# Kernel tuning notes

Measured on AMD Instinct MI355X. Metric: run time of the kernel, lower is better.

Reference implementation:

```python
import jax, jax.numpy as jnp
import numpy as np

THRESHOLD = 0.01
TOPK_RATIO = 0.7

def setup_inputs() -> dict:
    key = jax.random.key(0)
    k1, k2, k3, k4, k5 = jax.random.split(key, 5)
    B, N, F, K = 8, 2048, 512, 256
    x = jax.random.normal(k1, (B, N, F), dtype=jnp.float32)
    adj = jax.random.uniform(k2, (B, N, N), dtype=jnp.float32)
    mask = jnp.ones((B, N), dtype=jnp.float32)
    # assign_main = Linear(F->K), ReLU, Linear(K->K)
    W1 = jax.random.normal(k3, (F, K), dtype=jnp.float32) / np.sqrt(F)
    b1 = jnp.zeros((K,), dtype=jnp.float32)
    W2 = jax.random.normal(k4, (K, K), dtype=jnp.float32) / np.sqrt(K)
    b2 = jnp.zeros((K,), dtype=jnp.float32)
    return {"x": x, "adj": adj, "mask": mask, "W1": W1, "b1": b1, "W2": W2, "b2": b2}

def reference(x, adj, mask, W1, b1, W2, b2):
    B, N, Fdim = x.shape
    K = W2.shape[1]
    # soft assignment logits with masked softmax over clusters
    h = jax.nn.relu(jnp.einsum('bnf,fk->bnk', x, W1) + b1)
    logits = jnp.einsum('bnk,kl->bnl', h, W2) + b2            # [B,N,K]
    logits = logits + (-1e9) * (1.0 - mask[..., None])
    S = jax.nn.softmax(logits, axis=-1)                       # [B,N,K]
    # pooled features and pooled adjacency
    pfeat = jnp.einsum('bnk,bnf->bkf', S, x)                  # S^T x -> [B,K,F]
    mid = jnp.einsum('bnm,bmk->bnk', adj, S)                  # adj @ S
    pooled = jnp.einsum('bnk,bnl->bkl', S, mid)               # S^T adj S -> [B,K,K]
    # threshold + top-k sparsify with straight-through estimator
    topk = min(K, int(np.ceil(TOPK_RATIO * K)))
    thr_mask = (pooled >= THRESHOLD).astype(pooled.dtype)
    a_thr = pooled * thr_mask
    _, idx = jax.lax.top_k(a_thr, topk)                       # [B,K,topk]
    bi = jnp.arange(B)[:, None, None]
    ri = jnp.arange(K)[None, :, None]
    fmask = jnp.zeros_like(pooled).at[bi, ri, idx].set(1.0)
    a_sp = pooled * fmask
    a_ste = a_sp + jax.lax.stop_gradient(pooled - a_sp)       # forward == pooled
    # symmetric degree renormalization
    row_sum = a_ste.sum(axis=-1)
    d_inv_sqrt = 1.0 / jnp.sqrt(row_sum + 1e-9)
    pooled_adj = a_ste * d_inv_sqrt[:, :, None] * d_inv_sqrt[:, None, :]
    pmask = jnp.ones((B, K), dtype=x.dtype)
    return pfeat, pooled_adj, pmask
```

## Files before the change

kernel.cpp:

```cpp
#include <hip/hip_runtime.h>
#include <hip/hip_bf16.h>


typedef float f32x4 __attribute__((ext_vector_type(4)));
typedef __bf16 bf16x8 __attribute__((ext_vector_type(8)));

#define VMCNT(n) asm volatile("s_waitcnt vmcnt(" #n ")" ::: "memory")
#define LGKM0    asm volatile("s_waitcnt lgkmcnt(0)" ::: "memory")
#define SCHEDB   __builtin_amdgcn_sched_barrier(0)
#define BARRIER                                        \
  do {                                                 \
    LGKM0;                                             \
    __builtin_amdgcn_s_barrier();                      \
    asm volatile("" ::: "memory");                     \
    SCHEDB;                                            \
  } while (0)

__device__ __forceinline__ void async_load16(const void* g, void* l) {
  __builtin_amdgcn_global_load_lds((const __attribute__((address_space(1))) void*)g,
                                   (__attribute__((address_space(3))) void*)l, 16, 0, 0);
}
__device__ __forceinline__ unsigned short f2bf(float f) {
  return __builtin_bit_cast(unsigned short, (__bf16)f);
}
__device__ __forceinline__ ushort4 f4_to_bf4(float4 v) {
  ushort4 u; u.x = f2bf(v.x); u.y = f2bf(v.y); u.z = f2bf(v.z); u.w = f2bf(v.w); return u;
}

template <int ROWS, int BK, int NT>
__device__ __forceinline__ void stage_bf16(const __bf16* __restrict__ src, long long ld,
                                           __bf16* lds, int t) {
  constexpr int GR = BK / 8;
  constexpr int N = ROWS * GR / NT;
  static_assert(N >= 1, "stage too small");
#pragma unroll
  for (int c = 0; c < N; ++c) {
    const int idx = c * NT + t;
    const int row = idx / GR;
    const int g = idx % GR;
    const int gs = g ^ (row & (GR - 1) & 7);
    async_load16(src + (long long)row * ld + gs * 8, lds + idx * 8);
  }
}
template <int BK>
__device__ __forceinline__ bf16x8 frag(const __bf16* lds, int row, int kq) {
  constexpr int GR = BK / 8;
  const int g = kq ^ (row & (GR - 1) & 7);
  return *(const bf16x8*)(lds + row * BK + g * 8);
}

__global__ __launch_bounds__(256) void prep_k(const float* __restrict__ x,
                                              const float* __restrict__ W1,
                                              const float* __restrict__ W2,
                                              __bf16* __restrict__ xbT,
                                              __bf16* __restrict__ W1T,
                                              __bf16* __restrict__ W2T) {
  __shared__ float tile[64][65];
  const int tr = threadIdx.x >> 6, tc = threadIdx.x & 63;
  const int bid = blockIdx.x;
  const float* in; __bf16* out; int r0, c0, C, R;
  if (bid < 2048) {
    const int fb = bid >> 8, rest = bid & 255;
    const int nb = rest >> 3, b = rest & 7;
    in = x + (long long)b * 1048576; out = xbT + (long long)b * 1048576;
    r0 = nb * 64; c0 = fb * 64; R = 2048; C = 512;
  } else if (bid < 2080) {
    const int w = bid - 2048;
    in = W1; out = W1T; r0 = (w >> 2) * 64; c0 = (w & 3) * 64; R = 512; C = 256;
  } else {
    const int w = bid - 2080;
    in = W2; out = W2T; r0 = (w >> 2) * 64; c0 = (w & 3) * 64; R = 256; C = 256;
  }
#pragma unroll
  for (int i = 0; i < 16; ++i)
    tile[tr + i * 4][tc] = in[(long long)(r0 + tr + i * 4) * C + c0 + tc];
  __syncthreads();
#pragma unroll
  for (int i = 0; i < 16; ++i)
    out[(long long)(c0 + tr + i * 4) * R + r0 + tc] = (__bf16)tile[tc][tr + i * 4];
}

__device__ __forceinline__ void asg_compute(const __bf16* __restrict__ Abuf,
                                            const __bf16* __restrict__ Bbuf,
                                            f32x4 (&acc)[2][4], int wn, int l15, int l4) {
  bf16x8 af[2], bf[4];
#pragma unroll
  for (int i = 0; i < 2; ++i) af[i] = frag<32>(Abuf, i * 16 + l15, l4);
#pragma unroll
  for (int j = 0; j < 4; ++j) bf[j] = frag<32>(Bbuf, wn + j * 16 + l15, l4);
  __builtin_amdgcn_s_setprio(1);
#pragma unroll
  for (int i = 0; i < 2; ++i)
#pragma unroll
    for (int j = 0; j < 4; ++j)
      acc[i][j] = __builtin_amdgcn_mfma_f32_16x16x32_bf16(af[i], bf[j], acc[i][j], 0, 0, 0);
  __builtin_amdgcn_s_setprio(0);
}

__global__ __launch_bounds__(256) void assign_fused_k(
    const float* __restrict__ x, const __bf16* __restrict__ W1T,
    const __bf16* __restrict__ W2T, const float* __restrict__ b1,
    const float* __restrict__ b2, const float* __restrict__ mask,
    __bf16* __restrict__ ST) {
  __shared__ alignas(16) __bf16 Ax[2][32 * 32];
  __shared__ alignas(16) __bf16 Bw[2][256 * 32];
  __shared__ alignas(16) __bf16 hl[32 * 264];
  __shared__ float red[2][4][32];

  const int t = threadIdx.x;
  const int lane = t & 63, wave = t >> 6;
  const int l15 = lane & 15, l4 = lane >> 4;
  const int wn = wave * 64;
  const long long row0 = (long long)blockIdx.x * 32;
  const float* Xb = x + row0 * 512;

  const int arow = t >> 3, afq = t & 7;
  const int ag = afq >> 1;
  const int aoff = arow * 32 + ((ag ^ (arow & 3)) * 8) + (afq & 1) * 4;

  auto ldx = [&](int tile) -> float4 {
    return *(const float4*)(Xb + (long long)arow * 512 + tile * 32 + afq * 4);
  };
  auto sta = [&](__bf16* dst, float4 v) { *(ushort4*)&dst[aoff] = f4_to_bf4(v); };

  f32x4 acc[2][4] = {};

  float4 xA = ldx(0);
  SCHEDB;
  stage_bf16<256, 32, 256>(W1T, 512, Bw[0], t);
  SCHEDB;
  VMCNT(4); SCHEDB;
  sta(Ax[0], xA);
  float4 xB = ldx(1);
  SCHEDB;
  VMCNT(1); SCHEDB;
  BARRIER;

#pragma unroll 1
  for (int tt = 0; tt < 14; tt += 2) {
    stage_bf16<256, 32, 256>(W1T + (tt + 1) * 32, 512, Bw[1], t);
    SCHEDB;
    xA = ldx(tt + 2);
    SCHEDB;
    asg_compute(Ax[0], Bw[0], acc, wn, l15, l4);
    VMCNT(5); SCHEDB;
    sta(Ax[1], xB);
    VMCNT(1); SCHEDB;
    BARRIER;
    stage_bf16<256, 32, 256>(W1T + (tt + 2) * 32, 512, Bw[0], t);
    SCHEDB;
    xB = ldx(tt + 3);
    SCHEDB;
    asg_compute(Ax[1], Bw[1], acc, wn, l15, l4);
    VMCNT(5); SCHEDB;
    sta(Ax[0], xA);
    VMCNT(1); SCHEDB;
    BARRIER;
  }
  stage_bf16<256, 32, 256>(W1T + 15 * 32, 512, Bw[1], t);
  SCHEDB;
  asg_compute(Ax[0], Bw[0], acc, wn, l15, l4);
  VMCNT(4); SCHEDB;
  sta(Ax[1], xB);
  VMCNT(0); SCHEDB;
  BARRIER;
  asg_compute(Ax[1], Bw[1], acc, wn, l15, l4);

  stage_bf16<256, 32, 256>(W2T, 256, Bw[0], t);
  SCHEDB;
#pragma unroll
  for (int j = 0; j < 4; ++j) {
    const int col = wn + j * 16 + l15;
    const float bv = b1[col];
#pragma unroll
    for (int i = 0; i < 2; ++i)
#pragma unroll
      for (int r = 0; r < 4; ++r)
        hl[(i * 16 + l4 * 4 + r) * 264 + col] = (__bf16)fmaxf(acc[i][j][r] + bv, 0.f);
  }
  VMCNT(0); SCHEDB;
  BARRIER;

  f32x4 acc2[2][4] = {};
#pragma unroll 1
  for (int tt = 0; tt < 8; ++tt) {
    if (tt < 7) stage_bf16<256, 32, 256>(W2T + (tt + 1) * 32, 256, Bw[(tt & 1) ^ 1], t);
    SCHEDB;
    const __bf16* Bc = Bw[tt & 1];
    bf16x8 af[2], bf[4];
#pragma unroll
    for (int i = 0; i < 2; ++i)
      af[i] = *(const bf16x8*)(&hl[(i * 16 + l15) * 264 + tt * 32 + l4 * 8]);
#pragma unroll
    for (int j = 0; j < 4; ++j) bf[j] = frag<32>(Bc, wn + j * 16 + l15, l4);
#pragma unroll
    for (int i = 0; i < 2; ++i)
#pragma unroll
      for (int j = 0; j < 4; ++j)
        acc2[i][j] = __builtin_amdgcn_mfma_f32_16x16x32_bf16(af[i], bf[j], acc2[i][j], 0, 0, 0);
    VMCNT(0); SCHEDB;
    BARRIER;
  }

  float mb[2][4], mx[2][4], sm[2][4];
#pragma unroll
  for (int i = 0; i < 2; ++i)
#pragma unroll
    for (int r = 0; r < 4; ++r) {
      mb[i][r] = -1e9f * (1.0f - mask[row0 + i * 16 + l4 * 4 + r]);
      mx[i][r] = -3.4e38f;
      sm[i][r] = 0.f;
    }
#pragma unroll
  for (int j = 0; j < 4; ++j) {
    const float bv = b2[wn + j * 16 + l15];
#pragma unroll
    for (int i = 0; i < 2; ++i)
#pragma unroll
      for (int r = 0; r < 4; ++r) {
        const float v = acc2[i][j][r] + bv + mb[i][r];
        acc2[i][j][r] = v;
        mx[i][r] = fmaxf(mx[i][r], v);
      }
  }
#pragma unroll
  for (int i = 0; i < 2; ++i)
#pragma unroll
    for (int r = 0; r < 4; ++r) {
      float m = mx[i][r];
      m = fmaxf(m, __shfl_xor(m, 1, 64)); m = fmaxf(m, __shfl_xor(m, 2, 64));
      m = fmaxf(m, __shfl_xor(m, 4, 64)); m = fmaxf(m, __shfl_xor(m, 8, 64));
      mx[i][r] = m;
    }
  if (l15 == 0)
#pragma unroll
    for (int i = 0; i < 2; ++i)
#pragma unroll
      for (int r = 0; r < 4; ++r) red[0][wave][i * 16 + l4 * 4 + r] = mx[i][r];
  __syncthreads();
#pragma unroll
  for (int i = 0; i < 2; ++i)
#pragma unroll
    for (int r = 0; r < 4; ++r) {
      const int rl = i * 16 + l4 * 4 + r;
      mx[i][r] = fmaxf(fmaxf(red[0][0][rl], red[0][1][rl]),
                       fmaxf(red[0][2][rl], red[0][3][rl]));
    }
#pragma unroll
  for (int j = 0; j < 4; ++j)
#pragma unroll
    for (int i = 0; i < 2; ++i)
#pragma unroll
      for (int r = 0; r < 4; ++r) {
        const float e = __expf(acc2[i][j][r] - mx[i][r]);
        acc2[i][j][r] = e;
        sm[i][r] += e;
      }
#pragma unroll
  for (int i = 0; i < 2; ++i)
#pragma unroll
    for (int r = 0; r < 4; ++r) {
      float s = sm[i][r];
      s += __shfl_xor(s, 1, 64); s += __shfl_xor(s, 2, 64);
      s += __shfl_xor(s, 4, 64); s += __shfl_xor(s, 8, 64);
      sm[i][r] = s;
    }
  if (l15 == 0)
#pragma unroll
    for (int i = 0; i < 2; ++i)
#pragma unroll
      for (int r = 0; r < 4; ++r) red[1][wave][i * 16 + l4 * 4 + r] = sm[i][r];
  __syncthreads();
  float inv[2][4];
#pragma unroll
  for (int i = 0; i < 2; ++i)
#pragma unroll
    for (int r = 0; r < 4; ++r) {
      const int rl = i * 16 + l4 * 4 + r;
      inv[i][r] = 1.0f / (red[1][0][rl] + red[1][1][rl] + red[1][2][rl] + red[1][3][rl]);
    }
  const long long bb = row0 >> 11;
  const long long n0 = row0 & 2047;
  __bf16* Sb = ST + bb * 524288;
#pragma unroll
  for (int j = 0; j < 4; ++j) {
    const int col = wn + j * 16 + l15;
#pragma unroll
    for (int i = 0; i < 2; ++i) {
      ushort4 u;
      u.x = f2bf(acc2[i][j][0] * inv[i][0]);
      u.y = f2bf(acc2[i][j][1] * inv[i][1]);
      u.z = f2bf(acc2[i][j][2] * inv[i][2]);
      u.w = f2bf(acc2[i][j][3] * inv[i][3]);
      *(ushort4*)(Sb + (long long)col * 2048 + n0 + i * 16 + l4 * 4) = u;
    }
  }
}

__device__ __forceinline__ void adj_compute(const __bf16* __restrict__ Abuf,
                                            const __bf16* __restrict__ Bbuf,
                                            f32x4 (&acc)[2][4],
                                            int wn, int l15, int l4) {
#pragma unroll
  for (int ks = 0; ks < 2; ++ks) {
    bf16x8 af[2], bf[4];
#pragma unroll
    for (int i = 0; i < 2; ++i) af[i] = frag<64>(Abuf, i * 16 + l15, ks * 4 + l4);
#pragma unroll
    for (int j = 0; j < 4; ++j) bf[j] = frag<64>(Bbuf, wn + j * 16 + l15, ks * 4 + l4);
    __builtin_amdgcn_s_setprio(1);
#pragma unroll
    for (int i = 0; i < 2; ++i)
#pragma unroll
      for (int j = 0; j < 4; ++j)
        acc[i][j] = __builtin_amdgcn_mfma_f32_16x16x32_bf16(af[i], bf[j], acc[i][j], 0, 0, 0);
    __builtin_amdgcn_s_setprio(0);
  }
}

__global__ __launch_bounds__(256) void gemm_adj_k(const float* __restrict__ adj,
                                                  const __bf16* __restrict__ ST,
                                                  __bf16* __restrict__ midT) {
  __shared__ alignas(16) __bf16 Aa[2][32 * 64];
  __shared__ alignas(16) __bf16 Bs[2][256 * 64];
  const int t = threadIdx.x;
  const int lane = t & 63, wave = t >> 6;
  const int l15 = lane & 15, l4 = lane >> 4;
  const int wn = wave * 64;
  const int id = blockIdx.x;
  const int bz = id & 7;
  const long long r0 = (long long)(id >> 3) * 32;
  const float* Ab = adj + (long long)bz * 4194304 + r0 * 2048;
  const __bf16* Bb = ST + (long long)bz * 524288;

  const int arow = t >> 4, afq = t & 15;
  const int ag = afq >> 1;
  const int aoff0 = arow * 64 + ((ag ^ (arow & 7)) * 8) + (afq & 1) * 4;
  const int aoff1 = (arow + 16) * 64 + ((ag ^ ((arow + 16) & 7)) * 8) + (afq & 1) * 4;

  auto lda4 = [&](int tile, int half) -> float4 {
    return *(const float4*)(Ab + (long long)(arow + half * 16) * 2048 + tile * 64 + afq * 4);
  };
  auto sta = [&](__bf16* dst, float4 v0, float4 v1) {
    *(ushort4*)&dst[aoff0] = f4_to_bf4(v0);
    *(ushort4*)&dst[aoff1] = f4_to_bf4(v1);
  };

  f32x4 acc[2][4] = {};

  float4 aA0 = lda4(0, 0), aA1 = lda4(0, 1);
  SCHEDB;
  stage_bf16<256, 64, 256>(Bb, 2048, Bs[0], t);
  SCHEDB;
  VMCNT(8); SCHEDB;
  sta(Aa[0], aA0, aA1);
  float4 aB0 = lda4(1, 0), aB1 = lda4(1, 1);
  SCHEDB;
  VMCNT(2); SCHEDB;
  BARRIER;

#pragma unroll 1
  for (int tt = 0; tt < 30; tt += 2) {
    stage_bf16<256, 64, 256>(Bb + (tt + 1) * 64, 2048, Bs[1], t);
    SCHEDB;
    aA0 = lda4(tt + 2, 0); aA1 = lda4(tt + 2, 1);
    SCHEDB;
    adj_compute(Aa[0], Bs[0], acc, wn, l15, l4);
    VMCNT(10); SCHEDB;
    sta(Aa[1], aB0, aB1);
    VMCNT(2); SCHEDB;
    BARRIER;
    stage_bf16<256, 64, 256>(Bb + (tt + 2) * 64, 2048, Bs[0], t);
    SCHEDB;
    aB0 = lda4(tt + 3, 0); aB1 = lda4(tt + 3, 1);
    SCHEDB;
    adj_compute(Aa[1], Bs[1], acc, wn, l15, l4);
    VMCNT(10); SCHEDB;
    sta(Aa[0], aA0, aA1);
    VMCNT(2); SCHEDB;
    BARRIER;
  }
  stage_bf16<256, 64, 256>(Bb + 31 * 64, 2048, Bs[1], t);
  SCHEDB;
  adj_compute(Aa[0], Bs[0], acc, wn, l15, l4);
  VMCNT(8); SCHEDB;
  sta(Aa[1], aB0, aB1);
  VMCNT(0); SCHEDB;
  BARRIER;
  adj_compute(Aa[1], Bs[1], acc, wn, l15, l4);

  __bf16* Cb = midT + (long long)bz * 524288;
#pragma unroll
  for (int j = 0; j < 4; ++j) {
    const int l = wn + j * 16 + l15;
#pragma unroll
    for (int i = 0; i < 2; ++i) {
      ushort4 u;
      u.x = f2bf(acc[i][j][0]); u.y = f2bf(acc[i][j][1]);
      u.z = f2bf(acc[i][j][2]); u.w = f2bf(acc[i][j][3]);
      *(ushort4*)(Cb + (long long)l * 2048 + r0 + i * 16 + l4 * 4) = u;
    }
  }
}

__global__ __launch_bounds__(256) void gemm_feat_k(const __bf16* __restrict__ ST,
                                                   const __bf16* __restrict__ xbT,
                                                   float* __restrict__ pfeat) {
  __shared__ alignas(16) __bf16 As[2][32 * 64];
  __shared__ alignas(16) __bf16 Bs[2][64 * 64];
  const int t = threadIdx.x;
  const int lane = t & 63, wave = t >> 6;
  const int l15 = lane & 15, l4 = lane >> 4;
  const int wn = wave * 16;
  const int id = blockIdx.x;
  const int b = id & 7, j7 = id >> 3;
  const int kblk = j7 & 7, fblk = j7 >> 3;
  const __bf16* Ab = ST + (long long)b * 524288 + (long long)kblk * 32 * 2048;
  const __bf16* Bb = xbT + (long long)b * 1048576 + (long long)fblk * 64 * 2048;

  f32x4 acc[2] = {};
  stage_bf16<32, 64, 256>(Ab, 2048, As[0], t);
  stage_bf16<64, 64, 256>(Bb, 2048, Bs[0], t);
  __syncthreads();
#pragma unroll 1
  for (int tt = 0; tt < 32; ++tt) {
    const int cur = tt & 1;
    if (tt < 31) {
      stage_bf16<32, 64, 256>(Ab + (tt + 1) * 64, 2048, As[cur ^ 1], t);
      stage_bf16<64, 64, 256>(Bb + (tt + 1) * 64, 2048, Bs[cur ^ 1], t);
    }
#pragma unroll
    for (int ks = 0; ks < 2; ++ks) {
      bf16x8 af[2], bf;
#pragma unroll
      for (int i = 0; i < 2; ++i) af[i] = frag<64>(As[cur], i * 16 + l15, ks * 4 + l4);
      bf = frag<64>(Bs[cur], wn + l15, ks * 4 + l4);
#pragma unroll
      for (int i = 0; i < 2; ++i)
        acc[i] = __builtin_amdgcn_mfma_f32_16x16x32_bf16(af[i], bf, acc[i], 0, 0, 0);
    }
    __syncthreads();
  }
  float* out = pfeat + (long long)b * 131072;
#pragma unroll
  for (int i = 0; i < 2; ++i)
#pragma unroll
    for (int r = 0; r < 4; ++r)
      out[(long long)(kblk * 32 + i * 16 + l4 * 4 + r) * 512 + fblk * 64 + wn + l15] =
          acc[i][r];
}

__global__ __launch_bounds__(256) void gemm_pool_k(const __bf16* __restrict__ ST,
                                                   const __bf16* __restrict__ midT,
                                                   float* __restrict__ pooled) {
  __shared__ alignas(16) __bf16 As[2][32 * 64];
  __shared__ alignas(16) __bf16 Bs[2][32 * 64];
  const int t = threadIdx.x;
  const int lane = t & 63, wave = t >> 6;
  const int l15 = lane & 15, l4 = lane >> 4;
  const int wm = (wave >> 1) * 16, wn = (wave & 1) * 16;
  const int id = blockIdx.x;
  const int b = id & 7, j7 = id >> 3;
  const int kblk = j7 & 7, lblk = j7 >> 3;
  const __bf16* Ab = ST + (long long)b * 524288 + (long long)kblk * 32 * 2048;
  const __bf16* Bb = midT + (long long)b * 524288 + (long long)lblk * 32 * 2048;

  f32x4 acc = {};
  stage_bf16<32, 64, 256>(Ab, 2048, As[0], t);
  stage_bf16<32, 64, 256>(Bb, 2048, Bs[0], t);
  __syncthreads();
#pragma unroll 1
  for (int tt = 0; tt < 32; ++tt) {
    const int cur = tt & 1;
    if (tt < 31) {
      stage_bf16<32, 64, 256>(Ab + (tt + 1) * 64, 2048, As[cur ^ 1], t);
      stage_bf16<32, 64, 256>(Bb + (tt + 1) * 64, 2048, Bs[cur ^ 1], t);
    }
#pragma unroll
    for (int ks = 0; ks < 2; ++ks) {
      bf16x8 af = frag<64>(As[cur], wm + l15, ks * 4 + l4);
      bf16x8 bf = frag<64>(Bs[cur], wn + l15, ks * 4 + l4);
      acc = __builtin_amdgcn_mfma_f32_16x16x32_bf16(af, bf, acc, 0, 0, 0);
    }
    __syncthreads();
  }
  float* out = pooled + (long long)b * 65536;
#pragma unroll
  for (int r = 0; r < 4; ++r)
    out[(long long)(kblk * 32 + wm + l4 * 4 + r) * 256 + lblk * 32 + wn + l15] = acc[r];
}

__global__ __launch_bounds__(256) void rowsum_k(const float* __restrict__ pooled,
                                                float* __restrict__ dinv) {
  const int gr = blockIdx.x * 4 + (threadIdx.x >> 6);
  const int lane = threadIdx.x & 63;
  const float* p = pooled + (long long)gr * 256;
  float s = p[lane] + p[lane + 64] + p[lane + 128] + p[lane + 192];
#pragma unroll
  for (int o = 32; o > 0; o >>= 1) s += __shfl_xor(s, o, 64);
  if (lane == 0) dinv[gr] = rsqrtf(s + 1e-9f);
}

__global__ __launch_bounds__(256) void finalize_k(const float* __restrict__ pooled,
                                                  const float* __restrict__ dinv,
                                                  float* __restrict__ outAdj,
                                                  float* __restrict__ pmask) {
  const long long i = blockIdx.x * 256LL + threadIdx.x;
  const int c = (int)(i & 255);
  const int r = (int)((i >> 8) & 255);
  const int b = (int)(i >> 16);
  outAdj[i] = pooled[i] * dinv[b * 256 + r] * dinv[b * 256 + c];
  if (i < 2048) pmask[i] = 1.0f;
}

extern "C" void kernel_launch(void* const* d_in, const int* in_sizes, int n_in,
                              void* d_out, int out_size, void* d_ws, size_t ws_size,
                              hipStream_t stream) {
  (void)in_sizes; (void)n_in; (void)out_size; (void)ws_size;
  const float* x    = (const float*)d_in[0];
  const float* adj  = (const float*)d_in[1];
  const float* mask = (const float*)d_in[2];
  const float* W1   = (const float*)d_in[3];
  const float* b1   = (const float*)d_in[4];
  const float* W2   = (const float*)d_in[5];
  const float* b2   = (const float*)d_in[6];

  char* ws = (char*)d_ws;
  __bf16* ST     = (__bf16*)(ws + 0);
  __bf16* midT   = (__bf16*)(ws + 8388608);
  __bf16* xbT    = (__bf16*)(ws + 16777216);
  float*  pooled = (float*)(ws + 33554432);
  float*  dinv   = (float*)(ws + 35651584);
  __bf16* W1T    = (__bf16*)(ws + 35659776);
  __bf16* W2T    = (__bf16*)(ws + 35921920);

  float* pfeat  = (float*)d_out;
  float* outAdj = (float*)d_out + 1048576;
  float* pmask  = (float*)d_out + 1572864;

  prep_k<<<2096, 256, 0, stream>>>(x, W1, W2, xbT, W1T, W2T);
  assign_fused_k<<<512, 256, 0, stream>>>(x, W1T, W2T, b1, b2, mask, ST);
  gemm_feat_k<<<512, 256, 0, stream>>>(ST, xbT, pfeat);
  gemm_adj_k<<<512, 256, 0, stream>>>(adj, ST, midT);
  gemm_pool_k<<<512, 256, 0, stream>>>(ST, midT, pooled);
  rowsum_k<<<512, 256, 0, stream>>>(pooled, dinv);
  finalize_k<<<2048, 256, 0, stream>>>(pooled, dinv, outAdj, pmask);
}
```

Before: 113.4 us.

## Load adj GEMM B operand straight to registers; triple-buffer feat and pool GEMMs

In the adj@S kernel, the shared-memory staging of the 256x64 S tile is removed. Each wave now loads its B fragments straight from global memory into registers, double-buffered, and the wait and barrier order is adjusted. This cuts LDS traffic and shared-memory footprint, which could raise occupancy, but it adds register pressure and uncoalesced 16-byte global loads. The pfeat and pooled GEMM kernels move from double to triple LDS buffering, with vmcnt-based waits and fewer barriers, so loads run further ahead of compute.

```diff
diff --git a/kernel.cpp b/kernel.cpp
--- a/kernel.cpp
+++ b/kernel.cpp
@@ -297,23 +297,21 @@
   }
 }
 
-__device__ __forceinline__ void adj_compute(const __bf16* __restrict__ Abuf,
-                                            const __bf16* __restrict__ Bbuf,
-                                            f32x4 (&acc)[2][4],
-                                            int wn, int l15, int l4) {
+__device__ __forceinline__ void adj_cmp(const __bf16* __restrict__ Abuf,
+                                        const bf16x8* __restrict__ bq,
+                                        f32x4 (&acc)[2][4], int l15, int l4) {
 #pragma unroll
   for (int ks = 0; ks < 2; ++ks) {
-    bf16x8 af[2], bf[4];
+    bf16x8 af[2];
 #pragma unroll
     for (int i = 0; i < 2; ++i) af[i] = frag<64>(Abuf, i * 16 + l15, ks * 4 + l4);
-#pragma unroll
-    for (int j = 0; j < 4; ++j) bf[j] = frag<64>(Bbuf, wn + j * 16 + l15, ks * 4 + l4);
     __builtin_amdgcn_s_setprio(1);
 #pragma unroll
     for (int i = 0; i < 2; ++i)
 #pragma unroll
       for (int j = 0; j < 4; ++j)
-        acc[i][j] = __builtin_amdgcn_mfma_f32_16x16x32_bf16(af[i], bf[j], acc[i][j], 0, 0, 0);
+        acc[i][j] =
+            __builtin_amdgcn_mfma_f32_16x16x32_bf16(af[i], bq[j * 2 + ks], acc[i][j], 0, 0, 0);
     __builtin_amdgcn_s_setprio(0);
   }
 }
@@ -322,7 +320,6 @@
                                                   const __bf16* __restrict__ ST,
                                                   __bf16* __restrict__ midT) {
   __shared__ alignas(16) __bf16 Aa[2][32 * 64];
-  __shared__ alignas(16) __bf16 Bs[2][256 * 64];
   const int t = threadIdx.x;
   const int lane = t & 63, wave = t >> 6;
   const int l15 = lane & 15, l4 = lane >> 4;
@@ -345,49 +342,58 @@
     *(ushort4*)&dst[aoff0] = f4_to_bf4(v0);
     *(ushort4*)&dst[aoff1] = f4_to_bf4(v1);
   };
+  auto ldb = [&](bf16x8* dst, int tile) {
+#pragma unroll
+    for (int j = 0; j < 4; ++j)
+#pragma unroll
+      for (int ks = 0; ks < 2; ++ks)
+        dst[j * 2 + ks] = *(const bf16x8*)(Bb + (long long)(wn + j * 16 + l15) * 2048 +
+                                           tile * 64 + ks * 32 + l4 * 8);
+  };
 
   f32x4 acc[2][4] = {};
+  bf16x8 b0[8], b1[8];
 
   float4 aA0 = lda4(0, 0), aA1 = lda4(0, 1);
   SCHEDB;
-  stage_bf16<256, 64, 256>(Bb, 2048, Bs[0], t);
-  SCHEDB;
-  VMCNT(8); SCHEDB;
+  ldb(b0, 0);
+  SCHEDB;
+  float4 aB0 = lda4(1, 0), aB1 = lda4(1, 1);
+  SCHEDB;
+  VMCNT(10); SCHEDB;
   sta(Aa[0], aA0, aA1);
-  float4 aB0 = lda4(1, 0), aB1 = lda4(1, 1);
-  SCHEDB;
+  BARRIER;
   VMCNT(2); SCHEDB;
-  BARRIER;
 
 #pragma unroll 1
   for (int tt = 0; tt < 30; tt += 2) {
-    stage_bf16<256, 64, 256>(Bb + (tt + 1) * 64, 2048, Bs[1], t);
+    ldb(b1, tt + 1);
     SCHEDB;
     aA0 = lda4(tt + 2, 0); aA1 = lda4(tt + 2, 1);
     SCHEDB;
-    adj_compute(Aa[0], Bs[0], acc, wn, l15, l4);
+    adj_cmp(Aa[0], b0, acc, l15, l4);
     VMCNT(10); SCHEDB;
     sta(Aa[1], aB0, aB1);
+    BARRIER;
     VMCNT(2); SCHEDB;
-    BARRIER;
-    stage_bf16<256, 64, 256>(Bb + (tt + 2) * 64, 2048, Bs[0], t);
+    ldb(b0, tt + 2);
     SCHEDB;
     aB0 = lda4(tt + 3, 0); aB1 = lda4(tt + 3, 1);
     SCHEDB;
-    adj_compute(Aa[1], Bs[1], acc, wn, l15, l4);
+    adj_cmp(Aa[1], b1, acc, l15, l4);
     VMCNT(10); SCHEDB;
     sta(Aa[0], aA0, aA1);
+    BARRIER;
     VMCNT(2); SCHEDB;
-    BARRIER;
-  }
-  stage_bf16<256, 64, 256>(Bb + 31 * 64, 2048, Bs[1], t);
-  SCHEDB;
-  adj_compute(Aa[0], Bs[0], acc, wn, l15, l4);
+  }
+  ldb(b1, 31);
+  SCHEDB;
+  adj_cmp(Aa[0], b0, acc, l15, l4);
   VMCNT(8); SCHEDB;
   sta(Aa[1], aB0, aB1);
+  BARRIER;
   VMCNT(0); SCHEDB;
-  BARRIER;
-  adj_compute(Aa[1], Bs[1], acc, wn, l15, l4);
+  adj_cmp(Aa[1], b1, acc, l15, l4);
 
   __bf16* Cb = midT + (long long)bz * 524288;
 #pragma unroll
@@ -406,8 +412,8 @@
 __global__ __launch_bounds__(256) void gemm_feat_k(const __bf16* __restrict__ ST,
                                                    const __bf16* __restrict__ xbT,
                                                    float* __restrict__ pfeat) {
-  __shared__ alignas(16) __bf16 As[2][32 * 64];
-  __shared__ alignas(16) __bf16 Bs[2][64 * 64];
+  __shared__ alignas(16) __bf16 As[3][32 * 64];
+  __shared__ alignas(16) __bf16 Bs[3][64 * 64];
   const int t = threadIdx.x;
   const int lane = t & 63, wave = t >> 6;
   const int l15 = lane & 15, l4 = lane >> 4;
@@ -418,29 +424,50 @@
   const __bf16* Ab = ST + (long long)b * 524288 + (long long)kblk * 32 * 2048;
   const __bf16* Bb = xbT + (long long)b * 1048576 + (long long)fblk * 64 * 2048;
 
-  f32x4 acc[2] = {};
-  stage_bf16<32, 64, 256>(Ab, 2048, As[0], t);
-  stage_bf16<64, 64, 256>(Bb, 2048, Bs[0], t);
-  __syncthreads();
-#pragma unroll 1
-  for (int tt = 0; tt < 32; ++tt) {
-    const int cur = tt & 1;
-    if (tt < 31) {
-      stage_bf16<32, 64, 256>(Ab + (tt + 1) * 64, 2048, As[cur ^ 1], t);
-      stage_bf16<64, 64, 256>(Bb + (tt + 1) * 64, 2048, Bs[cur ^ 1], t);
-    }
+  auto stage = [&](int s, int buf) {
+    stage_bf16<32, 64, 256>(Ab + s * 64, 2048, (__bf16*)As + buf * 2048, t);
+    stage_bf16<64, 64, 256>(Bb + s * 64, 2048, (__bf16*)Bs + buf * 4096, t);
+  };
+  auto cmp = [&](int buf, f32x4 (&acc)[2]) {
+    const __bf16* Ac = (const __bf16*)As + buf * 2048;
+    const __bf16* Bc = (const __bf16*)Bs + buf * 4096;
 #pragma unroll
     for (int ks = 0; ks < 2; ++ks) {
       bf16x8 af[2], bf;
 #pragma unroll
-      for (int i = 0; i < 2; ++i) af[i] = frag<64>(As[cur], i * 16 + l15, ks * 4 + l4);
-      bf = frag<64>(Bs[cur], wn + l15, ks * 4 + l4);
+      for (int i = 0; i < 2; ++i) af[i] = frag<64>(Ac, i * 16 + l15, ks * 4 + l4);
+      bf = frag<64>(Bc, wn + l15, ks * 4 + l4);
 #pragma unroll
       for (int i = 0; i < 2; ++i)
         acc[i] = __builtin_amdgcn_mfma_f32_16x16x32_bf16(af[i], bf, acc[i], 0, 0, 0);
     }
-    __syncthreads();
-  }
+  };
+
+  f32x4 acc[2] = {};
+  stage(0, 0);
+  SCHEDB;
+  stage(1, 1);
+  SCHEDB;
+  VMCNT(3); SCHEDB;
+  BARRIER;
+
+  int cur = 0, stg = 2;
+#pragma unroll 1
+  for (int tt = 0; tt < 30; ++tt) {
+    stage(tt + 2, stg);
+    SCHEDB;
+    cmp(cur, acc);
+    VMCNT(3); SCHEDB;
+    BARRIER;
+    cur = (cur == 2) ? 0 : cur + 1;
+    stg = (stg == 2) ? 0 : stg + 1;
+  }
+  cmp(cur, acc);
+  VMCNT(0); SCHEDB;
+  BARRIER;
+  cur = (cur == 2) ? 0 : cur + 1;
+  cmp(cur, acc);
+
   float* out = pfeat + (long long)b * 131072;
 #pragma unroll
   for (int i = 0; i < 2; ++i)
@@ -453,8 +480,8 @@
 __global__ __launch_bounds__(256) void gemm_pool_k(const __bf16* __restrict__ ST,
                                                    const __bf16* __restrict__ midT,
                                                    float* __restrict__ pooled) {
-  __shared__ alignas(16) __bf16 As[2][32 * 64];
-  __shared__ alignas(16) __bf16 Bs[2][32 * 64];
+  __shared__ alignas(16) __bf16 As[3][32 * 64];
+  __shared__ alignas(16) __bf16 Bs[3][32 * 64];
   const int t = threadIdx.x;
   const int lane = t & 63, wave = t >> 6;
   const int l15 = lane & 15, l4 = lane >> 4;
@@ -465,25 +492,46 @@
   const __bf16* Ab = ST + (long long)b * 524288 + (long long)kblk * 32 * 2048;
   const __bf16* Bb = midT + (long long)b * 524288 + (long long)lblk * 32 * 2048;
 
+  auto stage = [&](int s, int buf) {
+    stage_bf16<32, 64, 256>(Ab + s * 64, 2048, (__bf16*)As + buf * 2048, t);
+    stage_bf16<32, 64, 256>(Bb + s * 64, 2048, (__bf16*)Bs + buf * 2048, t);
+  };
+  auto cmp = [&](int buf, f32x4& acc) {
+    const __bf16* Ac = (const __bf16*)As + buf * 2048;
+    const __bf16* Bc = (const __bf16*)Bs + buf * 2048;
+#pragma unroll
+    for (int ks = 0; ks < 2; ++ks) {
+      bf16x8 af = frag<64>(Ac, wm + l15, ks * 4 + l4);
+      bf16x8 bf = frag<64>(Bc, wn + l15, ks * 4 + l4);
+      acc = __builtin_amdgcn_mfma_f32_16x16x32_bf16(af, bf, acc, 0, 0, 0);
+    }
+  };
+
   f32x4 acc = {};
-  stage_bf16<32, 64, 256>(Ab, 2048, As[0], t);
-  stage_bf16<32, 64, 256>(Bb, 2048, Bs[0], t);
-  __syncthreads();
+  stage(0, 0);
+  SCHEDB;
+  stage(1, 1);
+  SCHEDB;
+  VMCNT(2); SCHEDB;
+  BARRIER;
+
+  int cur = 0, stg = 2;
 #pragma unroll 1
-  for (int tt = 0; tt < 32; ++tt) {
-    const int cur = tt & 1;
-    if (tt < 31) {
-      stage_bf16<32, 64, 256>(Ab + (tt + 1) * 64, 2048, As[cur ^ 1], t);
-      stage_bf16<32, 64, 256>(Bb + (tt + 1) * 64, 2048, Bs[cur ^ 1], t);
-    }
-#pragma unroll
-    for (int ks = 0; ks < 2; ++ks) {
-      bf16x8 af = frag<64>(As[cur], wm + l15, ks * 4 + l4);
-      bf16x8 bf = frag<64>(Bs[cur], wn + l15, ks * 4 + l4);
-      acc = __builtin_amdgcn_mfma_f32_16x16x32_bf16(af, bf, acc, 0, 0, 0);
-    }
-    __syncthreads();
-  }
+  for (int tt = 0; tt < 30; ++tt) {
+    stage(tt + 2, stg);
+    SCHEDB;
+    cmp(cur, acc);
+    VMCNT(2); SCHEDB;
+    BARRIER;
+    cur = (cur == 2) ? 0 : cur + 1;
+    stg = (stg == 2) ? 0 : stg + 1;
+  }
+  cmp(cur, acc);
+  VMCNT(0); SCHEDB;
+  BARRIER;
+  cur = (cur == 2) ? 0 : cur + 1;
+  cmp(cur, acc);
+
   float* out = pooled + (long long)b * 65536;
 #pragma unroll
   for (int r = 0; r < 4; ++r)
```

Measured after the change: 139.8 us. 1.23x slower.
